# Kernel tuning notes

Measured on AMD Instinct MI355X. Metric: run time of the kernel, lower is better.

The kernel has to match this reference:

```python
import jax, jax.numpy as jnp
import numpy as np

N_NODES = 100000
N_EDGES = 1600000
D_FEAT = 128
N_CLASSES = 10


def setup_inputs() -> dict:
    key = jax.random.key(0)
    ks = jax.random.split(key, 9)
    x = jax.random.normal(ks[0], (N_NODES, D_FEAT), dtype=jnp.float32)
    edge_src = jax.random.randint(ks[1], (N_EDGES,), 0, N_NODES, dtype=jnp.int32)
    edge_dst = jax.random.randint(ks[2], (N_EDGES,), 0, N_NODES, dtype=jnp.int32)
    s = 1.0 / np.sqrt(D_FEAT)
    W1 = jax.random.normal(ks[3], (D_FEAT, D_FEAT), dtype=jnp.float32) * s
    b1 = jax.random.normal(ks[4], (D_FEAT,), dtype=jnp.float32) * s
    W2 = jax.random.normal(ks[5], (D_FEAT, D_FEAT), dtype=jnp.float32) * s
    b2 = jax.random.normal(ks[6], (D_FEAT,), dtype=jnp.float32) * s
    W3 = jax.random.normal(ks[7], (D_FEAT, N_CLASSES), dtype=jnp.float32) * s
    b3 = jax.random.normal(ks[8], (N_CLASSES,), dtype=jnp.float32) * s
    return {"x": x, "edge_src": edge_src, "edge_dst": edge_dst,
            "W1": W1, "b1": b1, "W2": W2, "b2": b2, "W3": W3, "b3": b3}


def _neighbor_mean(x, src, dst, n_nodes):
    # scatter-mean of neighbor features; isolated nodes keep their own feature
    msg_sum = jax.ops.segment_sum(x[src], dst, num_segments=n_nodes)  # [N, D]
    deg = jax.ops.segment_sum(jnp.ones(src.shape, x.dtype), dst, num_segments=n_nodes)  # [N]
    mean = msg_sum / jnp.maximum(deg, 1.0)[:, None]
    return jnp.where(deg[:, None] > 0, mean, x)


def reference(x, edge_src, edge_dst, W1, b1, W2, b2, W3, b3):
    n = x.shape[0]
    # layer 1: aggregate -> linear -> tanh
    h = jnp.tanh(_neighbor_mean(x, edge_src, edge_dst, n) @ W1 + b1)
    # layer 2: aggregate -> linear -> tanh
    h = jnp.tanh(_neighbor_mean(h, edge_src, edge_dst, n) @ W2 + b2)
    # final linear head (no aggregation, no activation)
    logits = h @ W3 + b3
    return logits
```

## Files before the change

### kernel.cpp

```cpp
#include <hip/hip_runtime.h>

#define DF 128
#define AST 136
#define EPB 4096

typedef float f32x4 __attribute__((ext_vector_type(4)));
typedef short bf16x8 __attribute__((ext_vector_type(8)));

__device__ __forceinline__ ushort f2bf(float f) {
  union { float f; uint u; } c; c.f = f;
  uint u = c.u;
  uint r = (u + 0x7fffu + ((u >> 16) & 1u)) >> 16;
  return (ushort)r;
}
__device__ __forceinline__ float bf_lo(uint v) { union { uint u; float f; } c; c.u = v << 16; return c.f; }
__device__ __forceinline__ float bf_hi(uint v) { union { uint u; float f; } c; c.u = v & 0xffff0000u; return c.f; }

__device__ __forceinline__ void addv8(float* acc, uint4 v) {
  acc[0] += bf_lo(v.x); acc[1] += bf_hi(v.x);
  acc[2] += bf_lo(v.y); acc[3] += bf_hi(v.y);
  acc[4] += bf_lo(v.z); acc[5] += bf_hi(v.z);
  acc[6] += bf_lo(v.w); acc[7] += bf_hi(v.w);
}

__global__ void prep_hist_kernel(const int* __restrict__ dst, int* __restrict__ histG,
                                 int E, int nbuck, int nblocks,
                                 const float* __restrict__ x, ushort* __restrict__ xb,
                                 const float* __restrict__ W1, ushort* __restrict__ Wt1,
                                 const float* __restrict__ W2, ushort* __restrict__ Wt2,
                                 ushort* __restrict__ zbN, ushort* __restrict__ ybN, int n4) {
  __shared__ int lh[512];
  int tid = threadIdx.x;
  if ((int)blockIdx.x < nblocks) {
    int blk = blockIdx.x;
    for (int i = tid; i < nbuck; i += 256) lh[i] = 0;
    __syncthreads();
    int base = blk * EPB + tid * 4;
#pragma unroll
    for (int it = 0; it < EPB / 1024; ++it) {
      int e = base + it * 1024;
      if (e + 3 < E) {
        int4 d4 = *(const int4*)(dst + e);
        atomicAdd(&lh[d4.x >> 8], 1);
        atomicAdd(&lh[d4.y >> 8], 1);
        atomicAdd(&lh[d4.z >> 8], 1);
        atomicAdd(&lh[d4.w >> 8], 1);
      } else {
#pragma unroll
        for (int q = 0; q < 4; ++q) {
          int ee = e + q;
          if (ee < E) atomicAdd(&lh[dst[ee] >> 8], 1);
        }
      }
    }
    __syncthreads();
    for (int i = tid; i < nbuck; i += 256) histG[(size_t)i * nblocks + blk] = lh[i];
    return;
  }
  int i = ((int)blockIdx.x - nblocks) * 256 + tid;
  if (i < n4) {
    float4 v = ((const float4*)x)[i];
    ushort4 o; o.x = f2bf(v.x); o.y = f2bf(v.y); o.z = f2bf(v.z); o.w = f2bf(v.w);
    ((ushort4*)xb)[i] = o;
    return;
  }
  int j = i - n4;
  if (j < DF * DF) {
    int nr = j >> 7, k = j & 127;
    Wt1[j] = f2bf(W1[(size_t)k * DF + nr]);
    return;
  }
  j -= DF * DF;
  if (j < DF * DF) {
    int nr = j >> 7, k = j & 127;
    Wt2[j] = f2bf(W2[(size_t)k * DF + nr]);
    return;
  }
  j -= DF * DF;
  if (j < 16) { ((uint4*)zbN)[j] = (uint4){0, 0, 0, 0}; return; }
  j -= 16;
  if (j < 16) { ((uint4*)ybN)[j] = (uint4){0, 0, 0, 0}; }
}

__device__ __forceinline__ void gemm_tiles(const ushort* __restrict__ A,
                                           const ushort* __restrict__ Ws,
                                           ushort* __restrict__ out, int n, int ntiles,
                                           int tile0, int tstride, int tid) {
  int lane = tid & 63, w = tid >> 6;
  int wr = (w >> 1) * 32, wc = (w & 1) * 64;
  int r16 = lane & 15, g8 = (lane >> 4) * 8;
  for (int tile = tile0; tile < ntiles; tile += tstride) {
    int node0 = tile * 64;
    int ra = node0 + wr + r16;      if (ra >= n) ra = n - 1;
    int rb = node0 + wr + 16 + r16; if (rb >= n) rb = n - 1;
    const ushort* pa = A + (size_t)ra * DF + g8;
    const ushort* pb = A + (size_t)rb * DF + g8;

    f32x4 acc[2][4];
#pragma unroll
    for (int i = 0; i < 2; i++)
#pragma unroll
      for (int j = 0; j < 4; j++) acc[i][j] = (f32x4){0.f, 0.f, 0.f, 0.f};

#pragma unroll
    for (int ks = 0; ks < 4; ++ks) {
      bf16x8 a0 = *(const bf16x8*)(pa + ks * 32);
      bf16x8 a1 = *(const bf16x8*)(pb + ks * 32);
      int k0 = ks * 32 + g8;
#pragma unroll
      for (int j = 0; j < 4; j++) {
        bf16x8 b = *(const bf16x8*)&Ws[(wc + j * 16 + r16) * AST + k0];
        acc[0][j] = __builtin_amdgcn_mfma_f32_16x16x32_bf16(a0, b, acc[0][j], 0, 0, 0);
        acc[1][j] = __builtin_amdgcn_mfma_f32_16x16x32_bf16(a1, b, acc[1][j], 0, 0, 0);
      }
    }

#pragma unroll
    for (int mi = 0; mi < 2; mi++) {
#pragma unroll
      for (int j = 0; j < 4; j++) {
        int col = wc + j * 16 + r16;
        int rowb = wr + mi * 16 + (lane >> 4) * 4;
#pragma unroll
        for (int q = 0; q < 4; q++) {
          int node = node0 + rowb + q;
          if (node < n) out[(size_t)node * DF + col] = f2bf(acc[mi][j][q]);
        }
      }
    }
  }
}

__global__ __launch_bounds__(256) void scan1_gemm_kernel(
    const int* __restrict__ cnt, int* __restrict__ excl, int* __restrict__ bsums, int Mn,
    int nb_m, const ushort* __restrict__ xb, const ushort* __restrict__ Wt1,
    ushort* __restrict__ yb, int n, int ntiles) {
  __shared__ ushort Ws[128 * AST];
  __shared__ int wsum[4];
  int t = threadIdx.x;
  if ((int)blockIdx.x < nb_m) {
    int base = blockIdx.x * 1024 + t * 4;
    int v[4]; int s = 0;
#pragma unroll
    for (int i = 0; i < 4; i++) { int d = (base + i < Mn) ? cnt[base + i] : 0; v[i] = s; s += d; }
    int lane = t & 63, w = t >> 6;
    int sc = s;
#pragma unroll
    for (int off = 1; off < 64; off <<= 1) { int o = __shfl_up(sc, off); if (lane >= off) sc += o; }
    if (lane == 63) wsum[w] = sc;
    __syncthreads();
    int woff = 0;
    for (int i = 0; i < w; i++) woff += wsum[i];
    int toff = woff + (sc - s);
#pragma unroll
    for (int i = 0; i < 4; i++) if (base + i < Mn) excl[base + i] = toff + v[i];
    if (t == 255) bsums[blockIdx.x] = woff + sc;
    return;
  }
  for (int i = t; i < 128 * 16; i += 256) {
    int r = i >> 4, c = i & 15;
    uint4 v = ((const uint4*)(Wt1 + r * DF))[c];
    *(uint4*)&Ws[r * AST + c * 8] = v;
  }
  __syncthreads();
  gemm_tiles(xb, Ws, yb, n, ntiles, (int)blockIdx.x - nb_m, (int)gridDim.x - nb_m, t);
}

__global__ __launch_bounds__(256) void gemm_plain_kernel(
    const ushort* __restrict__ A, const ushort* __restrict__ Wt,
    ushort* __restrict__ out, int n, int ntiles) {
  __shared__ ushort Ws[128 * AST];
  int t = threadIdx.x;
  for (int i = t; i < 128 * 16; i += 256) {
    int r = i >> 4, c = i & 15;
    uint4 v = ((const uint4*)(Wt + r * DF))[c];
    *(uint4*)&Ws[r * AST + c * 8] = v;
  }
  __syncthreads();
  gemm_tiles(A, Ws, out, n, ntiles, blockIdx.x, gridDim.x, t);
}

__device__ __forceinline__ void scan_bsums_lds(const int* __restrict__ bsums, int nb,
                                               int* sbs, int* wsum) {
  int t = threadIdx.x;
  int v0 = (2 * t < nb) ? bsums[2 * t] : 0;
  int v1 = (2 * t + 1 < nb) ? bsums[2 * t + 1] : 0;
  int s = v0 + v1;
  int lane = t & 63, w = t >> 6;
  int sc = s;
#pragma unroll
  for (int off = 1; off < 64; off <<= 1) { int o = __shfl_up(sc, off); if (lane >= off) sc += o; }
  if (lane == 63) wsum[w] = sc;
  __syncthreads();
  int woff = 0;
  for (int i = 0; i < w; i++) woff += wsum[i];
  int excl = woff + sc - s;
  sbs[2 * t] = excl;
  sbs[2 * t + 1] = excl + v0;
  __syncthreads();
}

__global__ void bucket_scatter_kernel(const int* __restrict__ src, const int* __restrict__ dst,
                                      const int* __restrict__ histE, const int* __restrict__ bsums,
                                      int nb, uint* __restrict__ eb, int E, int nbuck, int nblocks) {
  __shared__ int lc[512];
  __shared__ int sbs[512];
  __shared__ int wsum[4];
  int tid = threadIdx.x, blk = blockIdx.x;
  scan_bsums_lds(bsums, nb, sbs, wsum);
  for (int i = tid; i < nbuck; i += 256) {
    int idx = i * nblocks + blk;
    lc[i] = histE[idx] + sbs[idx >> 10];
  }
  __syncthreads();
  int base = blk * EPB + tid * 4;
#pragma unroll
  for (int it = 0; it < EPB / 1024; ++it) {
    int e = base + it * 1024;
    if (e + 3 < E) {
      int4 s4 = *(const int4*)(src + e);
      int4 d4 = *(const int4*)(dst + e);
      int p0 = atomicAdd(&lc[d4.x >> 8], 1);
      eb[p0] = (uint)s4.x | ((uint)(d4.x & 255) << 24);
      int p1 = atomicAdd(&lc[d4.y >> 8], 1);
      eb[p1] = (uint)s4.y | ((uint)(d4.y & 255) << 24);
      int p2 = atomicAdd(&lc[d4.z >> 8], 1);
      eb[p2] = (uint)s4.z | ((uint)(d4.z & 255) << 24);
      int p3 = atomicAdd(&lc[d4.w >> 8], 1);
      eb[p3] = (uint)s4.w | ((uint)(d4.w & 255) << 24);
    } else {
#pragma unroll
      for (int q = 0; q < 4; ++q) {
        int ee = e + q;
        if (ee < E) {
          int d = dst[ee];
          int pos = atomicAdd(&lc[d >> 8], 1);
          eb[pos] = (uint)src[ee] | ((uint)(d & 255) << 24);
        }
      }
    }
  }
}

__global__ void bucket_sort_kernel(const uint* __restrict__ eb,
                                   const int* __restrict__ histE, const int* __restrict__ bsums,
                                   int nb, int* __restrict__ rowptr, int* __restrict__ csr,
                                   int N, int E, int nbuck, int nblocks) {
  __shared__ int cnt[256];
  __shared__ int cursor[256];
  __shared__ int sbs[512];
  __shared__ int wsum[4];
  int tid = threadIdx.x, b = blockIdx.x;
  scan_bsums_lds(bsums, nb, sbs, wsum);
  int idx = b * nblocks;
  int beg = histE[idx] + sbs[idx >> 10];
  int end = E;
  if (b + 1 < nbuck) { int i2 = (b + 1) * nblocks; end = histE[i2] + sbs[i2 >> 10]; }
  cnt[tid] = 0;
  __syncthreads();
  for (int e = beg + tid; e < end; e += 256)
    atomicAdd(&cnt[eb[e] >> 24], 1);
  __syncthreads();
  int v = cnt[tid];
  int lane = tid & 63, w = tid >> 6;
  int sc = v;
#pragma unroll
  for (int off = 1; off < 64; off <<= 1) { int o = __shfl_up(sc, off); if (lane >= off) sc += o; }
  if (lane == 63) wsum[w] = sc;
  __syncthreads();
  int woff = 0;
  for (int i = 0; i < w; i++) woff += wsum[i];
  int excl = woff + sc - v;
  int node = (b << 8) + tid;
  if (node <= N) rowptr[node] = beg + excl;
  cursor[tid] = beg + excl;
  __syncthreads();
  for (int e = beg + tid; e < end; e += 256) {
    uint vv = eb[e];
    int pos = atomicAdd(&cursor[vv >> 24], 1);
    csr[pos] = (int)(vv & 0x00FFFFFFu);
  }
}

__device__ __forceinline__ void gather_mean(const ushort* __restrict__ src,
                                            const int* __restrict__ rowptr,
                                            const int* __restrict__ csr,
                                            int node, int n, uint c16, float* acc) {
  int beg = rowptr[node], end = rowptr[node + 1];
  const char* xbase = (const char*)src;
#pragma unroll
  for (int i = 0; i < 8; i++) acc[i] = 0.f;
  int deg = end - beg;
  if (deg > 0) {
#pragma unroll 1
    for (int e = beg; e < end; e += 4) {
      int e1 = e + 1, e2 = e + 2, e3 = e + 3;
      uint r0 = (uint)csr[e];
      uint r1 = (e1 < end) ? (uint)csr[e1] : (uint)n;
      uint r2 = (e2 < end) ? (uint)csr[e2] : (uint)n;
      uint r3 = (e3 < end) ? (uint)csr[e3] : (uint)n;
      uint4 v0 = *(const uint4*)(xbase + (r0 * 256u + c16));
      uint4 v1 = *(const uint4*)(xbase + (r1 * 256u + c16));
      uint4 v2 = *(const uint4*)(xbase + (r2 * 256u + c16));
      uint4 v3 = *(const uint4*)(xbase + (r3 * 256u + c16));
      addv8(acc, v0);
      addv8(acc, v1);
      addv8(acc, v2);
      addv8(acc, v3);
    }
    float inv = 1.0f / (float)deg;
#pragma unroll
    for (int i = 0; i < 8; i++) acc[i] *= inv;
  } else {
    uint4 v = *(const uint4*)(xbase + ((uint)node * 256u + c16));
    float t[8] = {0, 0, 0, 0, 0, 0, 0, 0};
    addv8(t, v);
#pragma unroll
    for (int i = 0; i < 8; i++) acc[i] = t[i];
  }
}

__global__ __launch_bounds__(256) void agg_bias_tanh_kernel(
    const ushort* __restrict__ yb, const int* __restrict__ rowptr,
    const int* __restrict__ csr, const float* __restrict__ bias,
    ushort* __restrict__ h1, int n) {
  int tid = threadIdx.x;
  int node = (blockIdx.x * 256 + tid) >> 4;
  if (node >= n) return;
  uint c16 = (uint)(tid & 15) * 16u;
  float acc[8];
  gather_mean(yb, rowptr, csr, node, n, c16, acc);
  int d8 = (tid & 15) * 8;
  float4 bA = *(const float4*)(bias + d8);
  float4 bB = *(const float4*)(bias + d8 + 4);
  float h0 = tanhf(acc[0] + bA.x), hh1 = tanhf(acc[1] + bA.y);
  float h2 = tanhf(acc[2] + bA.z), h3 = tanhf(acc[3] + bA.w);
  float h4 = tanhf(acc[4] + bB.x), h5 = tanhf(acc[5] + bB.y);
  float h6 = tanhf(acc[6] + bB.z), h7 = tanhf(acc[7] + bB.w);
  uint4 r;
  r.x = (uint)f2bf(h0) | ((uint)f2bf(hh1) << 16);
  r.y = (uint)f2bf(h2) | ((uint)f2bf(h3) << 16);
  r.z = (uint)f2bf(h4) | ((uint)f2bf(h5) << 16);
  r.w = (uint)f2bf(h6) | ((uint)f2bf(h7) << 16);
  *(uint4*)((char*)h1 + ((uint)node * 256u + c16)) = r;
}

__global__ __launch_bounds__(256) void agg_head_kernel(
    const ushort* __restrict__ zb, const int* __restrict__ rowptr,
    const int* __restrict__ csr, const float* __restrict__ b2,
    const float* __restrict__ W3, const float* __restrict__ b3,
    float* __restrict__ out, int n) {
  __shared__ float W3s[DF * 10];
  int tid = threadIdx.x;
  for (int i = tid; i < DF * 10; i += 256) W3s[i] = W3[i];
  __syncthreads();
  int node = (blockIdx.x * 256 + tid) >> 4;
  if (node >= n) return;
  uint c16 = (uint)(tid & 15) * 16u;
  float acc[8];
  gather_mean(zb, rowptr, csr, node, n, c16, acc);
  int d8 = (tid & 15) * 8;
  float4 bA = *(const float4*)(b2 + d8);
  float4 bB = *(const float4*)(b2 + d8 + 4);
  float h[8];
  h[0] = tanhf(acc[0] + bA.x); h[1] = tanhf(acc[1] + bA.y);
  h[2] = tanhf(acc[2] + bA.z); h[3] = tanhf(acc[3] + bA.w);
  h[4] = tanhf(acc[4] + bB.x); h[5] = tanhf(acc[5] + bB.y);
  h[6] = tanhf(acc[6] + bB.z); h[7] = tanhf(acc[7] + bB.w);
  float part[10];
#pragma unroll
  for (int j = 0; j < 10; j++) part[j] = 0.f;
#pragma unroll
  for (int i = 0; i < 8; i++) {
    const float* wrow = &W3s[(d8 + i) * 10];
#pragma unroll
    for (int j = 0; j < 10; j++) part[j] += h[i] * wrow[j];
  }
#pragma unroll
  for (int j = 0; j < 10; j++) {
    part[j] += __shfl_xor(part[j], 1);
    part[j] += __shfl_xor(part[j], 2);
    part[j] += __shfl_xor(part[j], 4);
    part[j] += __shfl_xor(part[j], 8);
  }
  int l16 = tid & 15;
#pragma unroll
  for (int j = 0; j < 10; j++)
    if (l16 == j) out[(size_t)node * 10 + j] = part[j] + b3[j];
}

extern "C" void kernel_launch(void* const* d_in, const int* in_sizes, int n_in,
                              void* d_out, int out_size, void* d_ws, size_t ws_size,
                              hipStream_t stream) {
  const float* x    = (const float*)d_in[0];
  const int*   esrc = (const int*)d_in[1];
  const int*   edst = (const int*)d_in[2];
  const float* W1   = (const float*)d_in[3];
  const float* b1   = (const float*)d_in[4];
  const float* W2   = (const float*)d_in[5];
  const float* b2   = (const float*)d_in[6];
  const float* W3   = (const float*)d_in[7];
  const float* b3   = (const float*)d_in[8];
  float* out = (float*)d_out;

  const int N = in_sizes[0] / DF;
  const int E = in_sizes[1];

  const int nbuck   = (N + 255) >> 8;
  const int nblocks = (E + EPB - 1) / EPB;
  const int M = nbuck * nblocks;

  char* ws = (char*)d_ws;
  int*  rowptr = (int*)ws;
  int*  csr    = rowptr + (N + 1);
  int*  histG  = csr + E;
  int*  histE  = histG + M;
  int*  bsums2 = histE + M;
  uint* eb     = (uint*)(bsums2 + 1024);
  size_t off = (size_t)((char*)(eb + E) - ws);
  off = (off + 255) & ~(size_t)255;
  ushort* xb  = (ushort*)(ws + off);     off += (size_t)(N + 1) * DF * 2; off = (off + 255) & ~(size_t)255;
  ushort* Wt1 = (ushort*)(ws + off);     off += (size_t)DF * DF * 2;
  ushort* Wt2 = (ushort*)(ws + off);     off += (size_t)DF * DF * 2; off = (off + 255) & ~(size_t)255;
  ushort* yb  = (ushort*)(ws + off);     off += (size_t)(N + 1) * DF * 2; off = (off + 255) & ~(size_t)255;
  ushort* h1  = (ushort*)(ws + off);
  ushort* zb  = xb;

  int n4 = N * DF / 4;
  int prep_total = n4 + 2 * DF * DF + 32;
  int prep_blocks = (prep_total + 255) / 256;
  prep_hist_kernel<<<nblocks + prep_blocks, 256, 0, stream>>>(
      edst, histG, E, nbuck, nblocks,
      x, xb, W1, Wt1, W2, Wt2,
      xb + (size_t)N * DF, yb + (size_t)N * DF, n4);

  int nb_m = (M + 1023) / 1024;
  int ntiles = (N + 63) / 64;

  scan1_gemm_kernel<<<nb_m + 512, 256, 0, stream>>>(
      histG, histE, bsums2, M, nb_m, xb, Wt1, yb, N, ntiles);

  bucket_scatter_kernel<<<nblocks, 256, 0, stream>>>(esrc, edst, histE, bsums2, nb_m, eb, E, nbuck, nblocks);
  bucket_sort_kernel<<<nbuck, 256, 0, stream>>>(eb, histE, bsums2, nb_m, rowptr, csr, N, E, nbuck, nblocks);

  int agg_blocks = (N + 15) / 16;

  agg_bias_tanh_kernel<<<agg_blocks, 256, 0, stream>>>(yb, rowptr, csr, b1, h1, N);
  gemm_plain_kernel<<<512, 256, 0, stream>>>(h1, Wt2, zb, N, ntiles);
  agg_head_kernel<<<agg_blocks, 256, 0, stream>>>(zb, rowptr, csr, b2, W3, b3, out, N);
}
```

Baseline: 197.4 us.

## Move layer-1 GEMM into scatter kernel and use MFMA for output head

Splits the scan out into its own small kernel. The first-layer GEMM now runs as extra blocks inside the bucket-scatter kernel, so the heavy GEMM overlaps the atomic-bound scatter instead of the tiny scan. The final 128x10 head is recomputed with a bf16 MFMA over a per-block 16-node tile staged in LDS, replacing the per-thread FMAs and shuffle reductions. W3 is pre-transposed and padded to 16 rows in bf16 during prep. This rounds the layer-2 hidden state to bf16 before the head and adds a block-wide barrier in the aggregation kernel.

```diff
diff --git a/kernel.cpp b/kernel.cpp
--- a/kernel.cpp
+++ b/kernel.cpp
@@ -28,6 +28,7 @@
                                  const float* __restrict__ x, ushort* __restrict__ xb,
                                  const float* __restrict__ W1, ushort* __restrict__ Wt1,
                                  const float* __restrict__ W2, ushort* __restrict__ Wt2,
+                                 const float* __restrict__ W3, ushort* __restrict__ W3t,
                                  ushort* __restrict__ zbN, ushort* __restrict__ ybN, int n4) {
   __shared__ int lh[512];
   int tid = threadIdx.x;
@@ -77,9 +78,57 @@
     return;
   }
   j -= DF * DF;
+  if (j < 16 * DF) {
+    int nr = j >> 7, k = j & 127;
+    W3t[j] = (nr < 10) ? f2bf(W3[(size_t)k * 10 + nr]) : (ushort)0;
+    return;
+  }
+  j -= 16 * DF;
   if (j < 16) { ((uint4*)zbN)[j] = (uint4){0, 0, 0, 0}; return; }
   j -= 16;
   if (j < 16) { ((uint4*)ybN)[j] = (uint4){0, 0, 0, 0}; }
+}
+
+__global__ void scan1_kernel(const int* __restrict__ cnt, int* __restrict__ excl,
+                             int* __restrict__ bsums, int n) {
+  __shared__ int wsum[4];
+  int t = threadIdx.x;
+  int base = blockIdx.x * 1024 + t * 4;
+  int v[4]; int s = 0;
+#pragma unroll
+  for (int i = 0; i < 4; i++) { int d = (base + i < n) ? cnt[base + i] : 0; v[i] = s; s += d; }
+  int lane = t & 63, w = t >> 6;
+  int sc = s;
+#pragma unroll
+  for (int off = 1; off < 64; off <<= 1) { int o = __shfl_up(sc, off); if (lane >= off) sc += o; }
+  if (lane == 63) wsum[w] = sc;
+  __syncthreads();
+  int woff = 0;
+  for (int i = 0; i < w; i++) woff += wsum[i];
+  int toff = woff + (sc - s);
+#pragma unroll
+  for (int i = 0; i < 4; i++) if (base + i < n) excl[base + i] = toff + v[i];
+  if (t == 255) bsums[blockIdx.x] = woff + sc;
+}
+
+__device__ __forceinline__ void scan_bsums_lds(const int* __restrict__ bsums, int nb,
+                                               int* sbs, int* wsum) {
+  int t = threadIdx.x;
+  int v0 = (2 * t < nb) ? bsums[2 * t] : 0;
+  int v1 = (2 * t + 1 < nb) ? bsums[2 * t + 1] : 0;
+  int s = v0 + v1;
+  int lane = t & 63, w = t >> 6;
+  int sc = s;
+#pragma unroll
+  for (int off = 1; off < 64; off <<= 1) { int o = __shfl_up(sc, off); if (lane >= off) sc += o; }
+  if (lane == 63) wsum[w] = sc;
+  __syncthreads();
+  int woff = 0;
+  for (int i = 0; i < w; i++) woff += wsum[i];
+  int excl = woff + sc - s;
+  sbs[2 * t] = excl;
+  sbs[2 * t + 1] = excl + v0;
+  __syncthreads();
 }
 
 __device__ __forceinline__ void gemm_tiles(const ushort* __restrict__ A,
@@ -131,41 +180,6 @@
   }
 }
 
-__global__ __launch_bounds__(256) void scan1_gemm_kernel(
-    const int* __restrict__ cnt, int* __restrict__ excl, int* __restrict__ bsums, int Mn,
-    int nb_m, const ushort* __restrict__ xb, const ushort* __restrict__ Wt1,
-    ushort* __restrict__ yb, int n, int ntiles) {
-  __shared__ ushort Ws[128 * AST];
-  __shared__ int wsum[4];
-  int t = threadIdx.x;
-  if ((int)blockIdx.x < nb_m) {
-    int base = blockIdx.x * 1024 + t * 4;
-    int v[4]; int s = 0;
-#pragma unroll
-    for (int i = 0; i < 4; i++) { int d = (base + i < Mn) ? cnt[base + i] : 0; v[i] = s; s += d; }
-    int lane = t & 63, w = t >> 6;
-    int sc = s;
-#pragma unroll
-    for (int off = 1; off < 64; off <<= 1) { int o = __shfl_up(sc, off); if (lane >= off) sc += o; }
-    if (lane == 63) wsum[w] = sc;
-    __syncthreads();
-    int woff = 0;
-    for (int i = 0; i < w; i++) woff += wsum[i];
-    int toff = woff + (sc - s);
-#pragma unroll
-    for (int i = 0; i < 4; i++) if (base + i < Mn) excl[base + i] = toff + v[i];
-    if (t == 255) bsums[blockIdx.x] = woff + sc;
-    return;
-  }
-  for (int i = t; i < 128 * 16; i += 256) {
-    int r = i >> 4, c = i & 15;
-    uint4 v = ((const uint4*)(Wt1 + r * DF))[c];
-    *(uint4*)&Ws[r * AST + c * 8] = v;
-  }
-  __syncthreads();
-  gemm_tiles(xb, Ws, yb, n, ntiles, (int)blockIdx.x - nb_m, (int)gridDim.x - nb_m, t);
-}
-
 __global__ __launch_bounds__(256) void gemm_plain_kernel(
     const ushort* __restrict__ A, const ushort* __restrict__ Wt,
     ushort* __restrict__ out, int n, int ntiles) {
@@ -180,66 +194,61 @@
   gemm_tiles(A, Ws, out, n, ntiles, blockIdx.x, gridDim.x, t);
 }
 
-__device__ __forceinline__ void scan_bsums_lds(const int* __restrict__ bsums, int nb,
-                                               int* sbs, int* wsum) {
-  int t = threadIdx.x;
-  int v0 = (2 * t < nb) ? bsums[2 * t] : 0;
-  int v1 = (2 * t + 1 < nb) ? bsums[2 * t + 1] : 0;
-  int s = v0 + v1;
-  int lane = t & 63, w = t >> 6;
-  int sc = s;
-#pragma unroll
-  for (int off = 1; off < 64; off <<= 1) { int o = __shfl_up(sc, off); if (lane >= off) sc += o; }
-  if (lane == 63) wsum[w] = sc;
-  __syncthreads();
-  int woff = 0;
-  for (int i = 0; i < w; i++) woff += wsum[i];
-  int excl = woff + sc - s;
-  sbs[2 * t] = excl;
-  sbs[2 * t + 1] = excl + v0;
-  __syncthreads();
-}
-
-__global__ void bucket_scatter_kernel(const int* __restrict__ src, const int* __restrict__ dst,
-                                      const int* __restrict__ histE, const int* __restrict__ bsums,
-                                      int nb, uint* __restrict__ eb, int E, int nbuck, int nblocks) {
-  __shared__ int lc[512];
-  __shared__ int sbs[512];
-  __shared__ int wsum[4];
-  int tid = threadIdx.x, blk = blockIdx.x;
-  scan_bsums_lds(bsums, nb, sbs, wsum);
-  for (int i = tid; i < nbuck; i += 256) {
-    int idx = i * nblocks + blk;
-    lc[i] = histE[idx] + sbs[idx >> 10];
-  }
-  __syncthreads();
-  int base = blk * EPB + tid * 4;
-#pragma unroll
-  for (int it = 0; it < EPB / 1024; ++it) {
-    int e = base + it * 1024;
-    if (e + 3 < E) {
-      int4 s4 = *(const int4*)(src + e);
-      int4 d4 = *(const int4*)(dst + e);
-      int p0 = atomicAdd(&lc[d4.x >> 8], 1);
-      eb[p0] = (uint)s4.x | ((uint)(d4.x & 255) << 24);
-      int p1 = atomicAdd(&lc[d4.y >> 8], 1);
-      eb[p1] = (uint)s4.y | ((uint)(d4.y & 255) << 24);
-      int p2 = atomicAdd(&lc[d4.z >> 8], 1);
-      eb[p2] = (uint)s4.z | ((uint)(d4.z & 255) << 24);
-      int p3 = atomicAdd(&lc[d4.w >> 8], 1);
-      eb[p3] = (uint)s4.w | ((uint)(d4.w & 255) << 24);
-    } else {
-#pragma unroll
-      for (int q = 0; q < 4; ++q) {
-        int ee = e + q;
-        if (ee < E) {
-          int d = dst[ee];
-          int pos = atomicAdd(&lc[d >> 8], 1);
-          eb[pos] = (uint)src[ee] | ((uint)(d & 255) << 24);
+__global__ __launch_bounds__(256) void scatter_gemm_kernel(
+    const int* __restrict__ src, const int* __restrict__ dst,
+    const int* __restrict__ histE, const int* __restrict__ bsums, int nb,
+    uint* __restrict__ eb, int E, int nbuck, int nblocks,
+    const ushort* __restrict__ xb, const ushort* __restrict__ Wt1,
+    ushort* __restrict__ yb, int n, int ntiles) {
+  __shared__ __align__(16) ushort Ws[128 * AST];
+  int tid = threadIdx.x;
+  if ((int)blockIdx.x < nblocks) {
+    int* lc   = (int*)Ws;
+    int* sbs  = lc + 512;
+    int* wsum = sbs + 512;
+    int blk = blockIdx.x;
+    scan_bsums_lds(bsums, nb, sbs, wsum);
+    for (int i = tid; i < nbuck; i += 256) {
+      int idx = i * nblocks + blk;
+      lc[i] = histE[idx] + sbs[idx >> 10];
+    }
+    __syncthreads();
+    int base = blk * EPB + tid * 4;
+#pragma unroll
+    for (int it = 0; it < EPB / 1024; ++it) {
+      int e = base + it * 1024;
+      if (e + 3 < E) {
+        int4 s4 = *(const int4*)(src + e);
+        int4 d4 = *(const int4*)(dst + e);
+        int p0 = atomicAdd(&lc[d4.x >> 8], 1);
+        eb[p0] = (uint)s4.x | ((uint)(d4.x & 255) << 24);
+        int p1 = atomicAdd(&lc[d4.y >> 8], 1);
+        eb[p1] = (uint)s4.y | ((uint)(d4.y & 255) << 24);
+        int p2 = atomicAdd(&lc[d4.z >> 8], 1);
+        eb[p2] = (uint)s4.z | ((uint)(d4.z & 255) << 24);
+        int p3 = atomicAdd(&lc[d4.w >> 8], 1);
+        eb[p3] = (uint)s4.w | ((uint)(d4.w & 255) << 24);
+      } else {
+#pragma unroll
+        for (int q = 0; q < 4; ++q) {
+          int ee = e + q;
+          if (ee < E) {
+            int d = dst[ee];
+            int pos = atomicAdd(&lc[d >> 8], 1);
+            eb[pos] = (uint)src[ee] | ((uint)(d & 255) << 24);
+          }
         }
       }
     }
-  }
+    return;
+  }
+  for (int i = tid; i < 128 * 16; i += 256) {
+    int r = i >> 4, c = i & 15;
+    uint4 v = ((const uint4*)(Wt1 + r * DF))[c];
+    *(uint4*)&Ws[r * AST + c * 8] = v;
+  }
+  __syncthreads();
+  gemm_tiles(xb, Ws, yb, n, ntiles, (int)blockIdx.x - nblocks, (int)gridDim.x - nblocks, tid);
 }
 
 __global__ void bucket_sort_kernel(const uint* __restrict__ eb,
@@ -348,45 +357,58 @@
 __global__ __launch_bounds__(256) void agg_head_kernel(
     const ushort* __restrict__ zb, const int* __restrict__ rowptr,
     const int* __restrict__ csr, const float* __restrict__ b2,
-    const float* __restrict__ W3, const float* __restrict__ b3,
+    const ushort* __restrict__ W3t, const float* __restrict__ b3,
     float* __restrict__ out, int n) {
-  __shared__ float W3s[DF * 10];
+  __shared__ __align__(16) ushort Hs[16 * AST];
+  __shared__ __align__(16) ushort W3s[16 * AST];
   int tid = threadIdx.x;
-  for (int i = tid; i < DF * 10; i += 256) W3s[i] = W3[i];
-  __syncthreads();
+  {
+    int r = tid >> 4, c = tid & 15;
+    uint4 v = ((const uint4*)(W3t + r * DF))[c];
+    *(uint4*)&W3s[r * AST + c * 8] = v;
+  }
   int node = (blockIdx.x * 256 + tid) >> 4;
-  if (node >= n) return;
+  int node_ib = tid >> 4;
   uint c16 = (uint)(tid & 15) * 16u;
-  float acc[8];
-  gather_mean(zb, rowptr, csr, node, n, c16, acc);
-  int d8 = (tid & 15) * 8;
-  float4 bA = *(const float4*)(b2 + d8);
-  float4 bB = *(const float4*)(b2 + d8 + 4);
-  float h[8];
-  h[0] = tanhf(acc[0] + bA.x); h[1] = tanhf(acc[1] + bA.y);
-  h[2] = tanhf(acc[2] + bA.z); h[3] = tanhf(acc[3] + bA.w);
-  h[4] = tanhf(acc[4] + bB.x); h[5] = tanhf(acc[5] + bB.y);
-  h[6] = tanhf(acc[6] + bB.z); h[7] = tanhf(acc[7] + bB.w);
-  float part[10];
-#pragma unroll
-  for (int j = 0; j < 10; j++) part[j] = 0.f;
-#pragma unroll
-  for (int i = 0; i < 8; i++) {
-    const float* wrow = &W3s[(d8 + i) * 10];
-#pragma unroll
-    for (int j = 0; j < 10; j++) part[j] += h[i] * wrow[j];
-  }
-#pragma unroll
-  for (int j = 0; j < 10; j++) {
-    part[j] += __shfl_xor(part[j], 1);
-    part[j] += __shfl_xor(part[j], 2);
-    part[j] += __shfl_xor(part[j], 4);
-    part[j] += __shfl_xor(part[j], 8);
-  }
-  int l16 = tid & 15;
-#pragma unroll
-  for (int j = 0; j < 10; j++)
-    if (l16 == j) out[(size_t)node * 10 + j] = part[j] + b3[j];
+  bool active = node < n;
+  uint4 hr = (uint4){0, 0, 0, 0};
+  if (active) {
+    float acc[8];
+    gather_mean(zb, rowptr, csr, node, n, c16, acc);
+    int d8 = (tid & 15) * 8;
+    float4 bA = *(const float4*)(b2 + d8);
+    float4 bB = *(const float4*)(b2 + d8 + 4);
+    float h0 = tanhf(acc[0] + bA.x), h1 = tanhf(acc[1] + bA.y);
+    float h2 = tanhf(acc[2] + bA.z), h3 = tanhf(acc[3] + bA.w);
+    float h4 = tanhf(acc[4] + bB.x), h5 = tanhf(acc[5] + bB.y);
+    float h6 = tanhf(acc[6] + bB.z), h7 = tanhf(acc[7] + bB.w);
+    hr.x = (uint)f2bf(h0) | ((uint)f2bf(h1) << 16);
+    hr.y = (uint)f2bf(h2) | ((uint)f2bf(h3) << 16);
+    hr.z = (uint)f2bf(h4) | ((uint)f2bf(h5) << 16);
+    hr.w = (uint)f2bf(h6) | ((uint)f2bf(h7) << 16);
+  }
+  *(uint4*)&Hs[node_ib * AST + (tid & 15) * 8] = hr;
+  __syncthreads();
+
+  if (tid < 64) {
+    int l16 = tid & 15, g8 = (tid >> 4) * 8;
+    f32x4 acc = (f32x4){0.f, 0.f, 0.f, 0.f};
+#pragma unroll
+    for (int ks = 0; ks < 4; ++ks) {
+      bf16x8 a = *(const bf16x8*)&Hs[l16 * AST + ks * 32 + g8];
+      bf16x8 b = *(const bf16x8*)&W3s[l16 * AST + ks * 32 + g8];
+      acc = __builtin_amdgcn_mfma_f32_16x16x32_bf16(a, b, acc, 0, 0, 0);
+    }
+    if (l16 < 10) {
+      float bv = b3[l16];
+#pragma unroll
+      for (int q = 0; q < 4; ++q) {
+        int nib = (tid >> 4) * 4 + q;
+        int nd = blockIdx.x * 16 + nib;
+        if (nd < n) out[(size_t)nd * 10 + l16] = acc[q] + bv;
+      }
+    }
+  }
 }
 
 extern "C" void kernel_launch(void* const* d_in, const int* in_sizes, int n_in,
@@ -421,31 +443,34 @@
   off = (off + 255) & ~(size_t)255;
   ushort* xb  = (ushort*)(ws + off);     off += (size_t)(N + 1) * DF * 2; off = (off + 255) & ~(size_t)255;
   ushort* Wt1 = (ushort*)(ws + off);     off += (size_t)DF * DF * 2;
-  ushort* Wt2 = (ushort*)(ws + off);     off += (size_t)DF * DF * 2; off = (off + 255) & ~(size_t)255;
+  ushort* Wt2 = (ushort*)(ws + off);     off += (size_t)DF * DF * 2;
+  ushort* W3t = (ushort*)(ws + off);     off += (size_t)16 * DF * 2; off = (off + 255) & ~(size_t)255;
   ushort* yb  = (ushort*)(ws + off);     off += (size_t)(N + 1) * DF * 2; off = (off + 255) & ~(size_t)255;
   ushort* h1  = (ushort*)(ws + off);
   ushort* zb  = xb;
 
   int n4 = N * DF / 4;
-  int prep_total = n4 + 2 * DF * DF + 32;
+  int prep_total = n4 + 2 * DF * DF + 16 * DF + 32;
   int prep_blocks = (prep_total + 255) / 256;
   prep_hist_kernel<<<nblocks + prep_blocks, 256, 0, stream>>>(
       edst, histG, E, nbuck, nblocks,
-      x, xb, W1, Wt1, W2, Wt2,
+      x, xb, W1, Wt1, W2, Wt2, W3, W3t,
       xb + (size_t)N * DF, yb + (size_t)N * DF, n4);
 
   int nb_m = (M + 1023) / 1024;
   int ntiles = (N + 63) / 64;
 
-  scan1_gemm_kernel<<<nb_m + 512, 256, 0, stream>>>(
-      histG, histE, bsums2, M, nb_m, xb, Wt1, yb, N, ntiles);
-
-  bucket_scatter_kernel<<<nblocks, 256, 0, stream>>>(esrc, edst, histE, bsums2, nb_m, eb, E, nbuck, nblocks);
+  scan1_kernel<<<nb_m, 256, 0, stream>>>(histG, histE, bsums2, M);
+
+  scatter_gemm_kernel<<<nblocks + 512, 256, 0, stream>>>(
+      esrc, edst, histE, bsums2, nb_m, eb, E, nbuck, nblocks,
+      xb, Wt1, yb, N, ntiles);
+
   bucket_sort_kernel<<<nbuck, 256, 0, stream>>>(eb, histE, bsums2, nb_m, rowptr, csr, N, E, nbuck, nblocks);
 
   int agg_blocks = (N + 15) / 16;
 
   agg_bias_tanh_kernel<<<agg_blocks, 256, 0, stream>>>(yb, rowptr, csr, b1, h1, N);
   gemm_plain_kernel<<<512, 256, 0, stream>>>(h1, Wt2, zb, N, ntiles);
-  agg_head_kernel<<<agg_blocks, 256, 0, stream>>>(zb, rowptr, csr, b2, W3, b3, out, N);
-}
+  agg_head_kernel<<<agg_blocks, 256, 0, stream>>>(zb, rowptr, csr, b2, W3t, b3, out, N);
+}
```

Result: faster. 187.6 us (median of 2 runs) (-4.9%).
